# Kernel tuning notes

Measured on AMD Instinct MI355X. Metric: run time of the kernel, lower is better.

The kernel has to match this reference:

```python
import jax, jax.numpy as jnp
import numpy as np

N = 40000
E = 640000
IN = 128
H = 8
F = 16  # out_features per head; H*F == IN for the residual
NEG_SLOPE = 0.2
BN_EPS = 1e-5
SOFTMAX_EPS = 1e-16


def setup_inputs() -> dict:
    key = jax.random.key(0)
    ks = jax.random.split(key, 7)
    x = jax.random.normal(ks[0], (N, IN), dtype=jnp.float32)
    edge_index = jax.random.randint(ks[1], (2, E), 0, N, dtype=jnp.int32)
    # GATConv parameters (glorot-ish scale)
    W = jax.random.normal(ks[2], (IN, H * F), dtype=jnp.float32) * (1.0 / np.sqrt(IN))
    att_src = jax.random.normal(ks[3], (H, F), dtype=jnp.float32) * (1.0 / np.sqrt(F))
    att_dst = jax.random.normal(ks[4], (H, F), dtype=jnp.float32) * (1.0 / np.sqrt(F))
    bias = jnp.zeros((H * F,), dtype=jnp.float32)
    bn_gamma = jnp.ones((H * F,), dtype=jnp.float32)
    bn_beta = jnp.zeros((H * F,), dtype=jnp.float32)
    return {"x": x, "edge_index": edge_index, "W": W, "att_src": att_src,
            "att_dst": att_dst, "bias": bias, "bn_gamma": bn_gamma, "bn_beta": bn_beta}


def _gat_layer(x, src, dst, W, att_src, att_dst, bias, bn_gamma, bn_beta):
    n = x.shape[0]
    xp = (x @ W).reshape(n, H, F)                      # [N,H,F] transformed features
    a_s = jnp.einsum('nhf,hf->nh', xp, att_src)        # [N,H]
    a_d = jnp.einsum('nhf,hf->nh', xp, att_dst)
    e = jax.nn.leaky_relu(a_s[src] + a_d[dst], NEG_SLOPE)   # [E,H] per-edge logits
    # segment softmax over edges sharing the same destination node
    m = jax.ops.segment_max(e, dst, num_segments=n)    # [N,H]
    m = jnp.where(jnp.isfinite(m), m, 0.0)             # guard isolated nodes
    p = jnp.exp(e - m[dst])
    s = jax.ops.segment_sum(p, dst, num_segments=n)    # [N,H]
    alpha = p / (s[dst] + SOFTMAX_EPS)                 # [E,H]
    # scatter-aggregate messages
    msg = alpha[:, :, None] * xp[src]                  # [E,H,F]
    out = jax.ops.segment_sum(msg, dst, num_segments=n)  # [N,H,F]
    h = out.reshape(n, H * F) + bias
    # BatchNorm1d (training-mode batch statistics, biased variance)
    mean = h.mean(axis=0)
    var = h.var(axis=0)
    h = (h - mean) * jax.lax.rsqrt(var + BN_EPS) * bn_gamma + bn_beta
    h = jax.nn.relu(h)
    return h + x                                        # residual (dropout p=0 -> identity)


def reference(x, edge_index, W, att_src, att_dst, bias, bn_gamma, bn_beta):
    n = x.shape[0]
    loops = jnp.arange(n, dtype=edge_index.dtype)
    src = jnp.concatenate([edge_index[0], loops])       # add self-loops (GATConv default)
    dst = jnp.concatenate([edge_index[1], loops])
    return _gat_layer(x, src, dst, W, att_src, att_dst, bias, bn_gamma, bn_beta)
```

## Files before the change

### kernel.cpp

```cpp
#include <hip/hip_runtime.h>
#include <math.h>


constexpr float NEG_SLOPE = 0.2f;
constexpr float BN_EPS = 1e-5f;
constexpr float SM_EPS = 1e-16f;
constexpr int NBUCK = 640;
constexpr int IPB   = 8192;
constexpr int BCAP  = 1536;

typedef __attribute__((ext_vector_type(8))) short short8;
typedef __attribute__((ext_vector_type(4))) float f32x4;

__device__ inline unsigned bf16rne(float f) {
    unsigned b = __float_as_uint(f);
    return (b + 0x7fffu + ((b >> 16) & 1u)) >> 16;
}

__global__ __launch_bounds__(256) void k_init(
    const float* __restrict__ W, const float* __restrict__ att_src,
    const float* __restrict__ att_dst, unsigned short* __restrict__ Wtg,
    int* __restrict__ zbase, int zcount)
{
    int b = blockIdx.x;
    if (b < 64) {
        int idx = b * 256 + threadIdx.x;
        int k = idx >> 7, nc = idx & 127;
        Wtg[nc * 128 + k] = (unsigned short)bf16rne(W[idx]);
    } else if (b < 72) {
        int c = (b - 64) * 16 + (threadIdx.x >> 4);
        int j = threadIdx.x & 15;
        int h = j & 7;
        const float* att = (j < 8) ? att_src : att_dst;
        float v = 0.f;
#pragma unroll
        for (int f = 0; f < 16; ++f)
            v += W[c * 128 + h * 16 + f] * att[h * 16 + f];
        Wtg[(128 + j) * 128 + c] = (unsigned short)bf16rne(v);
    } else {
        int idx = (b - 72) * 256 + threadIdx.x;
        if (idx < zcount) zbase[idx] = 0;
    }
}

__global__ __launch_bounds__(256) void k_gemm(
    const float* __restrict__ x, const unsigned short* __restrict__ Wtg,
    const int* __restrict__ ei, int E,
    unsigned* __restrict__ xpb, float* __restrict__ a_s, float* __restrict__ a_d,
    int* __restrict__ bcur, unsigned* __restrict__ buck, int n,
    int ntiles)
{
    __shared__ int lh[NBUCK];
    __shared__ int cur[NBUCK];
    if ((int)blockIdx.x >= ntiles) {
        const int blkC = blockIdx.x - ntiles;
        const int T = E + n;
        for (int i = threadIdx.x; i < NBUCK; i += 256) lh[i] = 0;
        __syncthreads();
        const int base = blkC * IPB;
#pragma unroll
        for (int i = 0; i < IPB / 256; ++i) {
            int t = base + i * 256 + threadIdx.x;
            if (t < T) {
                int dst = (t < E) ? ei[E + t] : (t - E);
                atomicAdd(&lh[dst >> 6], 1);
            }
        }
        __syncthreads();
        for (int i = threadIdx.x; i < NBUCK; i += 256) {
            int c = lh[i];
            cur[i] = (c > 0) ? atomicAdd(&bcur[i], c) : 0;
        }
        __syncthreads();
#pragma unroll
        for (int i = 0; i < IPB / 256; ++i) {
            int t = base + i * 256 + threadIdx.x;
            if (t < T) {
                int dst, src;
                if (t < E) { dst = ei[E + t]; src = ei[t]; }
                else       { dst = src = t - E; }
                int bk = dst >> 6;
                int local = atomicAdd(&cur[bk], 1);
                if (local < BCAP)
                    buck[(size_t)bk * BCAP + local] =
                        ((unsigned)dst << 16) | (unsigned)src;
            }
        }
        return;
    }

    const int tid = threadIdx.x;
    const int lane = tid & 63;
    const int wid = tid >> 6;
    const int quad = lane >> 4;
    const int l16 = lane & 15;
    const int row = blockIdx.x * 64 + wid * 16 + l16;

    const float4* x4 = (const float4*)x;
    short8 afrag[4];
#pragma unroll
    for (int kt = 0; kt < 4; ++kt) {
        float4 f0 = make_float4(0.f, 0.f, 0.f, 0.f), f1 = f0;
        if (row < n) {
            f0 = x4[(size_t)row * 32 + kt * 8 + quad * 2];
            f1 = x4[(size_t)row * 32 + kt * 8 + quad * 2 + 1];
        }
        short8 a;
        a[0] = (short)bf16rne(f0.x); a[1] = (short)bf16rne(f0.y);
        a[2] = (short)bf16rne(f0.z); a[3] = (short)bf16rne(f0.w);
        a[4] = (short)bf16rne(f1.x); a[5] = (short)bf16rne(f1.y);
        a[6] = (short)bf16rne(f1.z); a[7] = (short)bf16rne(f1.w);
        afrag[kt] = a;
    }

    f32x4 acc[9];
#pragma unroll
    for (int ct = 0; ct < 9; ++ct) acc[ct] = (f32x4){0.f, 0.f, 0.f, 0.f};

#pragma unroll
    for (int ct = 0; ct < 9; ++ct) {
#pragma unroll
        for (int kt = 0; kt < 4; ++kt) {
            short8 bfr = *(const short8*)&Wtg[(size_t)(ct * 16 + l16) * 128 + kt * 32 + quad * 8];
            acc[ct] = __builtin_amdgcn_mfma_f32_16x16x32_bf16(afrag[kt], bfr, acc[ct], 0, 0, 0);
        }
    }

    const int rowbase = blockIdx.x * 64 + wid * 16 + quad * 4;
#pragma unroll
    for (int ct = 0; ct < 8; ++ct) {
#pragma unroll
        for (int r = 0; r < 4; ++r) {
            float val = acc[ct][r];
            float other = __shfl_xor(val, 1);
            int orow = rowbase + r;
            if (!(lane & 1) && orow < n) {
                unsigned u = bf16rne(val) | (bf16rne(other) << 16);
                xpb[(size_t)orow * 64 + ct * 8 + (l16 >> 1)] = u;
            }
        }
    }
#pragma unroll
    for (int r = 0; r < 4; ++r) {
        int orow = rowbase + r;
        if (orow < n) {
            float val = acc[8][r];
            if (l16 < 8) a_s[(size_t)orow * 8 + l16] = val;
            else         a_d[(size_t)orow * 8 + (l16 - 8)] = val;
        }
    }
}

__global__ __launch_bounds__(256) void k_bfin(
    const int* __restrict__ bcur, unsigned* __restrict__ buck,
    int* __restrict__ deg, int* __restrict__ rowst, int n)
{
    const int k = blockIdx.x;
    const int start = k * BCAP;
    const int cnt = min(bcur[k], BCAP);
    __shared__ unsigned it[BCAP];
    __shared__ unsigned so[BCAP];
    __shared__ int h[64], pf[64], curs[64];
    for (int i = threadIdx.x; i < cnt; i += 256) it[i] = buck[start + i];
    if (threadIdx.x < 64) h[threadIdx.x] = 0;
    __syncthreads();
    for (int i = threadIdx.x; i < cnt; i += 256)
        atomicAdd(&h[(it[i] >> 16) & 63], 1);
    __syncthreads();
    if (threadIdx.x < 64) {
        int p = 0;
        for (int j = 0; j < threadIdx.x; ++j) p += h[j];
        pf[threadIdx.x] = p;
        curs[threadIdx.x] = p;
    }
    __syncthreads();
    for (int i = threadIdx.x; i < cnt; i += 256) {
        unsigned v = it[i];
        int r = atomicAdd(&curs[(v >> 16) & 63], 1);
        so[r] = v;
    }
    __syncthreads();
    for (int i = threadIdx.x; i < cnt; i += 256) buck[start + i] = so[i];
    if (threadIdx.x < 64) {
        int dst = (k << 6) + threadIdx.x;
        if (dst < n) {
            deg[dst] = h[threadIdx.x];
            rowst[dst] = start + pf[threadIdx.x];
        }
    }
}

__global__ __launch_bounds__(256) void k_gather(
    const int* __restrict__ deg, const int* __restrict__ rowst,
    const unsigned* __restrict__ buck,
    const float* __restrict__ a_s, const float* __restrict__ a_d,
    const unsigned* __restrict__ xpb, unsigned* __restrict__ aggb, int n)
{
    int node = blockIdx.x * 4 + (threadIdx.x >> 6);
    if (node >= n) return;
    int lane = threadIdx.x & 63;
    int h = lane >> 3;
    float ad = a_d[(size_t)node * 8 + h];
    const unsigned* rowp = buck + rowst[node];
    int cnt = deg[node];
    float acc0 = 0.f, acc1 = 0.f, s = 0.f;

    for (int slot = 0; slot < cnt; slot += 8) {
        int sx[8]; float w[8]; unsigned u[8];
#pragma unroll
        for (int j = 0; j < 8; ++j) {
            int sj = slot + j;
            sx[j] = (int)(rowp[sj < cnt ? sj : cnt - 1] & 0xffffu);
        }
#pragma unroll
        for (int j = 0; j < 8; ++j) w[j] = a_s[(size_t)sx[j] * 8 + h];
#pragma unroll
        for (int j = 0; j < 8; ++j) u[j] = xpb[(size_t)sx[j] * 64 + lane];
#pragma unroll
        for (int j = 0; j < 8; ++j) {
            float v = w[j] + ad;
            v = v > 0.f ? v : NEG_SLOPE * v;
            float p = __expf(v);
            p = (slot + j < cnt) ? p : 0.f;
            s += p;
            acc0 = fmaf(p, __uint_as_float(u[j] << 16), acc0);
            acc1 = fmaf(p, __uint_as_float(u[j] & 0xffff0000u), acc1);
        }
    }
    float inv = 1.0f / (s + SM_EPS);
    aggb[(size_t)node * 64 + lane] = bf16rne(acc0 * inv) | (bf16rne(acc1 * inv) << 16);
}

__global__ __launch_bounds__(256) void k_bnstats(
    const unsigned* __restrict__ aggb, int n, float* __restrict__ stats)
{
    __shared__ float red[4][256];
    const int cp = threadIdx.x & 63;
    const int rg = threadIdx.x >> 6;
    float s0 = 0.f, s1 = 0.f, q0 = 0.f, q1 = 0.f;
    for (int r = blockIdx.x * 4 + rg; r < n; r += gridDim.x * 4) {
        unsigned u = aggb[(size_t)r * 64 + cp];
        float v0 = __uint_as_float(u << 16);
        float v1 = __uint_as_float(u & 0xffff0000u);
        s0 += v0; q0 += v0 * v0;
        s1 += v1; q1 += v1 * v1;
    }
    red[rg][cp * 2] = s0;       red[rg][cp * 2 + 1] = s1;
    red[rg][128 + cp * 2] = q0; red[rg][128 + cp * 2 + 1] = q1;
    __syncthreads();
    int idx = threadIdx.x;
    float v = red[0][idx] + red[1][idx] + red[2][idx] + red[3][idx];
    if (idx < 128) atomicAdd(&stats[idx], v);
    else           atomicAdd(&stats[128 + (idx - 128)], v);
}

__global__ __launch_bounds__(256) void k_final(
    const unsigned* __restrict__ aggb, const float* __restrict__ gamma,
    const float* __restrict__ beta, const float* __restrict__ stats,
    const float* __restrict__ x, float* __restrict__ out, int n)
{
    int i4 = blockIdx.x * 256 + threadIdx.x;
    int total4 = n * 32;
    if (i4 >= total4) return;
    int c4 = (i4 & 31) * 4;
    float invn = 1.0f / (float)n;
    uint2 au = ((const uint2*)aggb)[i4];
    float av[4] = { __uint_as_float(au.x << 16), __uint_as_float(au.x & 0xffff0000u),
                    __uint_as_float(au.y << 16), __uint_as_float(au.y & 0xffff0000u) };
    float4 xv = ((const float4*)x)[i4];
    float4 o;
#pragma unroll
    for (int j = 0; j < 4; ++j) {
        int c = c4 + j;
        float mean = stats[c] * invn;
        float var = stats[128 + c] * invn - mean * mean;
        float v = (av[j] - mean) * rsqrtf(var + BN_EPS) * gamma[c] + beta[c];
        v = fmaxf(v, 0.f);
        (&o.x)[j] = v + (&xv.x)[j];
    }
    ((float4*)out)[i4] = o;
}

extern "C" void kernel_launch(void* const* d_in, const int* in_sizes, int n_in,
                              void* d_out, int out_size, void* d_ws, size_t ws_size,
                              hipStream_t stream)
{
    const float* x        = (const float*)d_in[0];
    const int*   ei       = (const int*)d_in[1];
    const float* W        = (const float*)d_in[2];
    const float* att_src  = (const float*)d_in[3];
    const float* att_dst  = (const float*)d_in[4];
    const float* bn_gamma = (const float*)d_in[6];
    const float* bn_beta  = (const float*)d_in[7];
    float* out = (float*)d_out;

    const int n = in_sizes[0] / 128;
    const int E = in_sizes[1] / 2;
    const int T = E + n;
    const int nba = (T + IPB - 1) / IPB;

    float*          stats = (float*)d_ws;
    int*            bcur  = (int*)(stats + 256);
    int*            deg   = bcur + NBUCK;
    int*            rowst = deg + n;
    unsigned short* Wtg   = (unsigned short*)(rowst + n);
    unsigned*       xpb   = (unsigned*)(Wtg + 144 * 128);
    unsigned*       aggb  = xpb + (size_t)n * 64;
    float*          a_s   = (float*)(aggb + (size_t)n * 64);
    float*          a_d   = a_s + (size_t)n * 8;
    unsigned*       buck  = (unsigned*)(a_d + (size_t)n * 8);

    const int zcount = 256 + NBUCK + n;
    const int ginit = 72 + (zcount + 255) / 256;
    const int ntiles = (n + 63) >> 6;
    const int ggemm = ntiles + nba;

    k_init<<<ginit, 256, 0, stream>>>(W, att_src, att_dst, Wtg,
                                      (int*)stats, zcount);
    k_gemm<<<ggemm, 256, 0, stream>>>(x, Wtg, ei, E, xpb, a_s, a_d,
                                      bcur, buck, n, ntiles);
    k_bfin<<<NBUCK, 256, 0, stream>>>(bcur, buck, deg, rowst, n);
    k_gather<<<(n + 3) / 4, 256, 0, stream>>>(deg, rowst, buck, a_s, a_d,
                                              xpb, aggb, n);
    k_bnstats<<<640, 256, 0, stream>>>(aggb, n, stats);
    k_final<<<(n * 32 + 255) / 256, 256, 0, stream>>>(aggb, bn_gamma, bn_beta,
                                                      stats, x, out, n);
}
```

Baseline: 181.0 us.

## Stage bucketed edges in LDS and write them out contiguously per bucket

The edge-bucketing blocks now compute a local prefix sum over bucket counts, scatter packed edges into a shared-memory staging array sorted by bucket, and then stream them to global buckets in order. Consecutive threads therefore write consecutive addresses within each bucket, replacing scattered 4-byte global stores. This adds 32KB of LDS plus extra barriers and a serial 64-entry scan. The shared allocation is also declared in the GEMM path, which may lower occupancy for the GEMM tiles.

```diff
diff --git a/kernel.cpp b/kernel.cpp
--- a/kernel.cpp
+++ b/kernel.cpp
@@ -50,41 +50,76 @@
     int* __restrict__ bcur, unsigned* __restrict__ buck, int n,
     int ntiles)
 {
-    __shared__ int lh[NBUCK];
-    __shared__ int cur[NBUCK];
+    __shared__ int cnt[NBUCK];
+    __shared__ int off[NBUCK];
+    __shared__ int cur2[NBUCK];
+    __shared__ unsigned stg[IPB];
+    __shared__ int part[64];
+    __shared__ int tot;
+
     if ((int)blockIdx.x >= ntiles) {
+        const int tid = threadIdx.x;
         const int blkC = blockIdx.x - ntiles;
         const int T = E + n;
-        for (int i = threadIdx.x; i < NBUCK; i += 256) lh[i] = 0;
+        for (int i = tid; i < NBUCK; i += 256) cnt[i] = 0;
         __syncthreads();
         const int base = blkC * IPB;
 #pragma unroll
         for (int i = 0; i < IPB / 256; ++i) {
-            int t = base + i * 256 + threadIdx.x;
+            int t = base + i * 256 + tid;
             if (t < T) {
                 int dst = (t < E) ? ei[E + t] : (t - E);
-                atomicAdd(&lh[dst >> 6], 1);
+                atomicAdd(&cnt[dst >> 6], 1);
             }
         }
         __syncthreads();
-        for (int i = threadIdx.x; i < NBUCK; i += 256) {
-            int c = lh[i];
-            cur[i] = (c > 0) ? atomicAdd(&bcur[i], c) : 0;
+        if (tid < 64) {
+            int s = 0;
+#pragma unroll
+            for (int j = 0; j < 10; ++j) s += cnt[tid * 10 + j];
+            part[tid] = s;
+        }
+        __syncthreads();
+        if (tid == 0) {
+            int run = 0;
+#pragma unroll
+            for (int j = 0; j < 64; ++j) { int v = part[j]; part[j] = run; run += v; }
+            tot = run;
+        }
+        __syncthreads();
+        if (tid < 64) {
+            int run = part[tid];
+#pragma unroll
+            for (int j = 0; j < 10; ++j) {
+                int k = tid * 10 + j;
+                off[k] = run; cur2[k] = run; run += cnt[k];
+            }
+        }
+        __syncthreads();
+        for (int i = tid; i < NBUCK; i += 256) {
+            int c = cnt[i];
+            cnt[i] = (c > 0) ? atomicAdd(&bcur[i], c) : 0;
         }
         __syncthreads();
 #pragma unroll
         for (int i = 0; i < IPB / 256; ++i) {
-            int t = base + i * 256 + threadIdx.x;
+            int t = base + i * 256 + tid;
             if (t < T) {
                 int dst, src;
                 if (t < E) { dst = ei[E + t]; src = ei[t]; }
                 else       { dst = src = t - E; }
                 int bk = dst >> 6;
-                int local = atomicAdd(&cur[bk], 1);
-                if (local < BCAP)
-                    buck[(size_t)bk * BCAP + local] =
-                        ((unsigned)dst << 16) | (unsigned)src;
+                int r = atomicAdd(&cur2[bk], 1);
+                stg[r] = ((unsigned)dst << 16) | (unsigned)src;
             }
+        }
+        __syncthreads();
+        for (int i = tid; i < tot; i += 256) {
+            unsigned v = stg[i];
+            int bk = v >> 22;
+            int pos = cnt[bk] + (i - off[bk]);
+            if (pos < BCAP)
+                buck[(size_t)bk * BCAP + pos] = v;
         }
         return;
     }
```

Result: no change. 179.9 us (-0.6%).
